# Performance work log

Hardware: AMD Instinct MI355X
Metric: run time of the kernel (lower is better)

Reference implementation:

```python
import jax, jax.numpy as jnp
import numpy as np

B_, C_, H_, W_, N_ = 2, 256, 64, 64, 16


def setup_inputs() -> dict:
    key = jax.random.key(0)
    ks = jax.random.split(key, 6)
    return {
        "features": jax.random.normal(ks[0], (B_, C_, H_, W_), jnp.float32),
        "A_log": jax.random.normal(ks[1], (C_, N_), jnp.float32) * 0.5,
        "D": jax.random.normal(ks[2], (C_,), jnp.float32),
        "W_delta": jax.random.normal(ks[3], (C_, C_), jnp.float32) * 0.02,
        "b_delta": jnp.zeros((C_,), jnp.float32),
        "W_B": jax.random.normal(ks[4], (C_, N_), jnp.float32) * 0.02,
        "W_C": jax.random.normal(ks[5], (C_, N_), jnp.float32) * 0.02,
    }


def _selective_scan(x, A_log, D, W_delta, b_delta, W_B, W_C):
    # x: (B, L, C) -> (B, L, C). Canonical S6 selective scan (mamba corrector).
    delta = jax.nn.softplus(x @ W_delta + b_delta)          # (B, L, C)
    Bm = x @ W_B                                            # (B, L, N)
    Cm = x @ W_C                                            # (B, L, N)
    A = -jnp.exp(A_log)                                     # (C, N), negative real
    dA = jnp.exp(delta[..., None] * A)                      # (B, L, C, N)
    dBx = (delta * x)[..., None] * Bm[:, :, None, :]        # (B, L, C, N)

    def combine(left, right):
        a_l, b_l = left
        a_r, b_r = right
        return (a_l * a_r, a_r * b_l + b_r)

    # h_t = dA_t * h_{t-1} + dBx_t, computed in parallel over L
    _, h = jax.lax.associative_scan(combine, (dA, dBx), axis=1)
    y = jnp.einsum('blcn,bln->blc', h, Cm) + x * D          # (B, L, C)
    return y


def reference(features, A_log, D, W_delta, b_delta, W_B, W_C):
    B, C, H, W = features.shape
    corr = lambda x: _selective_scan(x, A_log, D, W_delta, b_delta, W_B, W_C)

    # direction 1: row-major forward
    flat = features.reshape(B, C, H * W).transpose(0, 2, 1)        # (B, HW, C)
    out1 = corr(flat)
    # direction 2: row-major reversed
    out2 = jnp.flip(corr(jnp.flip(flat, axis=1)), axis=1)
    # direction 3: rows flipped vertically (flip over H), scan, flip back
    rows = features.transpose(0, 2, 3, 1)                          # (B, H, W, C)
    rows_f = jnp.flip(rows, axis=1).reshape(B, H * W, C)
    out3 = jnp.flip(corr(rows_f).reshape(B, H, W, C), axis=1).reshape(B, H * W, C)
    # direction 4: column-major, flipped over W, scan, flip + transpose back
    cols = features.transpose(0, 3, 2, 1)                          # (B, W, H, C)
    cols_f = jnp.flip(cols, axis=1).reshape(B, W * H, C)
    out4 = jnp.flip(corr(cols_f).reshape(B, W, H, C), axis=1)
    out4 = out4.transpose(0, 2, 1, 3).reshape(B, H * W, C)

    mamba_out = (out1 + out2 + out3 + out4) / 4                    # (B, HW, C)
    return mamba_out.transpose(0, 2, 1).reshape(B, C, H, W)
```

## Files before the change

### kernel.cpp

```cpp
#include <hip/hip_runtime.h>
#include <cstdint>
#include <cstddef>

#define BB 2
#define CC 256
#define NN 16
#define LL 4096
#define NCH 128
#define CLEN 32
#define LCH 8
#define LOG2E 1.4426950408889634f

__device__ __forceinline__ float softplus_f(float z) {
    return fmaxf(z, 0.f) + log1pf(expf(-fabsf(z)));
}

__global__ __launch_bounds__(256) void k1_delta_gemm(
    const float* __restrict__ feat, const float* __restrict__ Wd,
    const float* __restrict__ bd, const float* __restrict__ WB,
    const float* __restrict__ WC, float* __restrict__ du,
    float* __restrict__ Bm, float* __restrict__ Cm)
{
    int lc = blockIdx.x & 511;
    int b  = blockIdx.x >> 9;
    int l0 = lc * LCH;
    int c  = threadIdx.x;
    const float* fbase = feat + (size_t)b * CC * LL;

    int lB  = threadIdx.x >> 5;
    int s   = threadIdx.x & 31;
    int mat = s >> 4;
    int n   = s & 15;
    const float* wBC = mat ? WC : WB;

    float accM[LCH] = {};
    float accB = 0.f;

    #pragma unroll 4
    for (int k = 0; k < 256; ++k) {
        const float* frow = fbase + (size_t)k * LL + l0;
        float4 x0 = *(const float4*)(frow + 0);
        float4 x1 = *(const float4*)(frow + 4);
        float wv = Wd[(size_t)k * CC + c];
        float wb = wBC[k * NN + n];
        float xb = frow[lB];

        accM[0] = fmaf(x0.x, wv, accM[0]);
        accM[1] = fmaf(x0.y, wv, accM[1]);
        accM[2] = fmaf(x0.z, wv, accM[2]);
        accM[3] = fmaf(x0.w, wv, accM[3]);
        accM[4] = fmaf(x1.x, wv, accM[4]);
        accM[5] = fmaf(x1.y, wv, accM[5]);
        accM[6] = fmaf(x1.z, wv, accM[6]);
        accM[7] = fmaf(x1.w, wv, accM[7]);
        accB = fmaf(xb, wb, accB);
    }

    (mat ? Cm : Bm)[((size_t)b * LL + l0 + lB) * NN + n] = accB;

    float bdc = bd[c];
    float4 fx[2];
    {
        const float* fcp = fbase + (size_t)c * LL + l0;
        fx[0] = *(const float4*)(fcp + 0);
        fx[1] = *(const float4*)(fcp + 4);
    }
    float2* du2 = (float2*)du;
    const float* fxs = (const float*)fx;
    #pragma unroll
    for (int j = 0; j < LCH; ++j) {
        float dv = softplus_f(accM[j] + bdc);
        float uv = dv * fxs[j];
        du2[((size_t)b * LL + l0 + j) * CC + c] = make_float2(dv, uv);
    }
}

__global__ __launch_bounds__(256) void p1_aggr(
    const float2* __restrict__ du, const float* __restrict__ Bm,
    const float* __restrict__ A_log, float* __restrict__ P, float* __restrict__ S)
{
    int blk = blockIdx.x;
    int cls = blk >> 8;
    int b   = (blk >> 7) & 1;
    int ch  = blk & 127;
    int p0, inner;
    if (cls == 0)      { p0 = 32 * ch;        inner = 1; }
    else if (cls == 1) { p0 = 4095 - 32 * ch; inner = -1; }
    else               { p0 = 63 - (ch >> 1) + 2048 * (ch & 1); inner = 64; }
    int c = threadIdx.x;
    __shared__ float sBm[CLEN * NN];
    for (int i = threadIdx.x; i < CLEN * NN; i += 256) {
        int j = i >> 4, nn = i & 15;
        sBm[i] = Bm[((size_t)b * LL + (p0 + inner * j)) * NN + nn];
    }
    float A2[NN];
    {
        const float4* al = (const float4*)(A_log + c * NN);
        #pragma unroll
        for (int q = 0; q < 4; ++q) {
            float4 v = al[q];
            A2[q*4+0] = -expf(v.x) * LOG2E;
            A2[q*4+1] = -expf(v.y) * LOG2E;
            A2[q*4+2] = -expf(v.z) * LOG2E;
            A2[q*4+3] = -expf(v.w) * LOG2E;
        }
    }
    __syncthreads();
    const float2* dub = du + (size_t)b * LL * CC + c;
    float2 buf[2][8];
    #pragma unroll
    for (int i = 0; i < 8; ++i)
        buf[0][i] = dub[(size_t)(p0 + inner * i) * CC];
    float Sv[NN] = {};
    float sumd = 0.f;
    #pragma unroll
    for (int g = 0; g < 4; ++g) {
        if (g < 3) {
            #pragma unroll
            for (int i = 0; i < 8; ++i)
                buf[(g + 1) & 1][i] = dub[(size_t)(p0 + inner * ((g + 1) * 8 + i)) * CC];
        }
        #pragma unroll
        for (int i = 0; i < 8; ++i) {
            int j = g * 8 + i;
            float2 dv = buf[g & 1][i];
            sumd += dv.x;
            float dA[NN];
            #pragma unroll
            for (int nn = 0; nn < NN; ++nn) dA[nn] = __builtin_amdgcn_exp2f(A2[nn] * dv.x);
            #pragma unroll
            for (int nn = 0; nn < NN; ++nn)
                Sv[nn] = fmaf(dA[nn], Sv[nn], dv.y * sBm[j * 16 + nn]);
        }
    }
    size_t base = ((size_t)((cls * 2 + b) * 128 + ch)) * 4096 + (size_t)c * 16;
    #pragma unroll
    for (int nn = 0; nn < NN; ++nn) {
        P[base + nn] = __builtin_amdgcn_exp2f(A2[nn] * sumd);
        S[base + nn] = Sv[nn];
    }
}

__global__ __launch_bounds__(128) void p2_scan(
    const float* __restrict__ P, const float* __restrict__ S, float* __restrict__ Hin)
{
    int r = blockIdx.x * 128 + threadIdx.x;
    int cn = r & 4095;
    int db = r >> 12;
    int d = db >> 1;
    int cls = (d == 1) ? 1 : ((d == 3) ? 2 : 0);
    int b = db & 1;
    const size_t cbase = ((size_t)(cls * 2 + b) * 128) * 4096 + cn;
    const size_t obase = ((size_t)db * 128) * 4096 + cn;
    float h = 0.f;
    for (int g = 0; g < 16; ++g) {
        float pv[8], sv[8];
        #pragma unroll
        for (int i = 0; i < 8; ++i) {
            int ch = g * 8 + i;
            int chm = (d == 2) ? (126 - 2 * (ch >> 1) + (ch & 1)) : ch;
            size_t ix = cbase + (size_t)chm * 4096;
            pv[i] = P[ix];
            sv[i] = S[ix];
        }
        #pragma unroll
        for (int i = 0; i < 8; ++i) {
            Hin[obase + (size_t)(g * 8 + i) * 4096] = h;
            h = fmaf(pv[i], h, sv[i]);
        }
    }
}

__global__ __launch_bounds__(256) void p3_replay(
    const float2* __restrict__ du, const float* __restrict__ Bm,
    const float* __restrict__ Cm, const float* __restrict__ A_log,
    const float* __restrict__ Hin, float* __restrict__ yA,
    float* __restrict__ yB, float* __restrict__ yC)
{
    int blk = blockIdx.x;
    int sec = blk >> 8;
    int b   = (blk >> 7) & 1;
    int ch  = blk & 127;
    int p0, inner;
    if (sec == 0)      { p0 = 32 * ch;        inner = 1; }
    else if (sec == 1) { p0 = 4095 - 32 * ch; inner = -1; }
    else               { p0 = 63 - (ch >> 1) + 2048 * (ch & 1); inner = 64; }
    int c = threadIdx.x;
    __shared__ float sBm[CLEN * NN];
    __shared__ float sCm[CLEN * NN];
    for (int i = threadIdx.x; i < CLEN * NN; i += 256) {
        int j = i >> 4, nn = i & 15;
        size_t o = ((size_t)b * LL + (p0 + inner * j)) * NN + nn;
        sBm[i] = Bm[o];
        sCm[i] = Cm[o];
    }
    float A2[NN];
    {
        const float4* al = (const float4*)(A_log + c * NN);
        #pragma unroll
        for (int q = 0; q < 4; ++q) {
            float4 v = al[q];
            A2[q*4+0] = -expf(v.x) * LOG2E;
            A2[q*4+1] = -expf(v.y) * LOG2E;
            A2[q*4+2] = -expf(v.z) * LOG2E;
            A2[q*4+3] = -expf(v.w) * LOG2E;
        }
    }
    const float2* dub = du + (size_t)b * LL * CC + c;

    if (sec == 0) {
        int ch2 = 126 - (ch & ~1) + (ch & 1);
        float h0[NN], h2[NN];
        {
            const float4* hp0 = (const float4*)(Hin + ((size_t)(0 * 2 + b) * 128 + ch)  * 4096 + (size_t)c * 16);
            const float4* hp2 = (const float4*)(Hin + ((size_t)(2 * 2 + b) * 128 + ch2) * 4096 + (size_t)c * 16);
            #pragma unroll
            for (int q = 0; q < 4; ++q) {
                float4 v0 = hp0[q], v2 = hp2[q];
                h0[q*4+0]=v0.x; h0[q*4+1]=v0.y; h0[q*4+2]=v0.z; h0[q*4+3]=v0.w;
                h2[q*4+0]=v2.x; h2[q*4+1]=v2.y; h2[q*4+2]=v2.z; h2[q*4+3]=v2.w;
            }
        }
        __syncthreads();
        float2 buf[2][8];
        #pragma unroll
        for (int i = 0; i < 8; ++i)
            buf[0][i] = dub[(size_t)(p0 + i) * CC];
        #pragma unroll
        for (int g = 0; g < 4; ++g) {
            if (g < 3) {
                #pragma unroll
                for (int i = 0; i < 8; ++i)
                    buf[(g + 1) & 1][i] = dub[(size_t)(p0 + (g + 1) * 8 + i) * CC];
            }
            #pragma unroll
            for (int i = 0; i < 8; ++i) {
                int j = g * 8 + i;
                float2 dv = buf[g & 1][i];
                float dA[NN];
                #pragma unroll
                for (int nn = 0; nn < NN; ++nn) dA[nn] = __builtin_amdgcn_exp2f(A2[nn] * dv.x);
                float y0v = 0.f, y2v = 0.f;
                #pragma unroll
                for (int nn = 0; nn < NN; ++nn) {
                    float Bu = dv.y * sBm[j * 16 + nn];
                    float cm = sCm[j * 16 + nn];
                    h0[nn] = fmaf(dA[nn], h0[nn], Bu);
                    h2[nn] = fmaf(dA[nn], h2[nn], Bu);
                    y0v = fmaf(h0[nn], cm, y0v);
                    y2v = fmaf(h2[nn], cm, y2v);
                }
                yA[((size_t)b * LL + p0 + j) * CC + c] = 0.25f * (y0v + y2v);
            }
        }
    } else {
        int d = (sec == 1) ? 1 : 3;
        float h[NN];
        {
            const float4* hp = (const float4*)(Hin + ((size_t)(d * 2 + b) * 128 + ch) * 4096 + (size_t)c * 16);
            #pragma unroll
            for (int q = 0; q < 4; ++q) {
                float4 v = hp[q];
                h[q*4+0]=v.x; h[q*4+1]=v.y; h[q*4+2]=v.z; h[q*4+3]=v.w;
            }
        }
        __syncthreads();
        float* yD = (sec == 1) ? yB : yC;
        float2 buf[2][8];
        #pragma unroll
        for (int i = 0; i < 8; ++i)
            buf[0][i] = dub[(size_t)(p0 + inner * i) * CC];
        #pragma unroll
        for (int g = 0; g < 4; ++g) {
            if (g < 3) {
                #pragma unroll
                for (int i = 0; i < 8; ++i)
                    buf[(g + 1) & 1][i] = dub[(size_t)(p0 + inner * ((g + 1) * 8 + i)) * CC];
            }
            #pragma unroll
            for (int i = 0; i < 8; ++i) {
                int j = g * 8 + i;
                float2 dv = buf[g & 1][i];
                float dA[NN];
                #pragma unroll
                for (int nn = 0; nn < NN; ++nn) dA[nn] = __builtin_amdgcn_exp2f(A2[nn] * dv.x);
                float yv = 0.f;
                #pragma unroll
                for (int nn = 0; nn < NN; ++nn) {
                    float Bu = dv.y * sBm[j * 16 + nn];
                    h[nn] = fmaf(dA[nn], h[nn], Bu);
                    yv = fmaf(h[nn], sCm[j * 16 + nn], yv);
                }
                yD[((size_t)b * LL + p0 + inner * j) * CC + c] = 0.25f * yv;
            }
        }
    }
}

__global__ __launch_bounds__(256) void k6_reduce(
    const float* __restrict__ feat, const float* __restrict__ D,
    const float* __restrict__ yA, const float* __restrict__ yB,
    const float* __restrict__ yC, float* __restrict__ out)
{
    int pt = blockIdx.x & 63;
    int ct = (blockIdx.x >> 6) & 3;
    int b  = blockIdx.x >> 8;
    int p0 = pt * 64, c0 = ct * 64;
    __shared__ float tile[64 * 65];
    {
        int cl = threadIdx.x & 63;
        int pg = threadIdx.x >> 6;
        #pragma unroll
        for (int pp = 0; pp < 16; ++pp) {
            int pl = pp * 4 + pg;
            size_t ix = ((size_t)b * LL + p0 + pl) * CC + c0 + cl;
            tile[cl * 65 + pl] = yA[ix] + yB[ix] + yC[ix];
        }
    }
    __syncthreads();
    {
        int pl = threadIdx.x & 63;
        int cg = threadIdx.x >> 6;
        #pragma unroll
        for (int cc = 0; cc < 16; ++cc) {
            int cloc = cc * 4 + cg;
            int c = c0 + cloc;
            size_t o = ((size_t)b * CC + c) * LL + p0 + pl;
            out[o] = tile[cloc * 65 + pl] + feat[o] * D[c];
        }
    }
}

extern "C" void kernel_launch(void* const* d_in, const int* in_sizes, int n_in,
                              void* d_out, int out_size, void* d_ws, size_t ws_size,
                              hipStream_t stream)
{
    const float* feat  = (const float*)d_in[0];
    const float* A_log = (const float*)d_in[1];
    const float* D     = (const float*)d_in[2];
    const float* Wd    = (const float*)d_in[3];
    const float* bd    = (const float*)d_in[4];
    const float* WB    = (const float*)d_in[5];
    const float* WC    = (const float*)d_in[6];
    float* out = (float*)d_out;

    float* ws  = (float*)d_ws;
    float* du  = ws;
    float* Bm  = du  + (size_t)4194304;
    float* Cm  = Bm  + (size_t)131072;
    float* P   = Cm  + (size_t)131072;
    float* S   = P   + (size_t)3145728;
    float* Hin = S   + (size_t)3145728;
    float* yA  = Hin + (size_t)4194304;
    float* yB  = yA  + (size_t)2097152;
    float* yC  = yB  + (size_t)2097152;

    k1_delta_gemm<<<1024, 256, 0, stream>>>(feat, Wd, bd, WB, WC, du, Bm, Cm);
    p1_aggr<<<768, 256, 0, stream>>>((const float2*)du, Bm, A_log, P, S);
    p2_scan<<<256, 128, 0, stream>>>(P, S, Hin);
    p3_replay<<<768, 256, 0, stream>>>((const float2*)du, Bm, Cm, A_log, Hin, yA, yB, yC);
    k6_reduce<<<512, 256, 0, stream>>>(feat, D, yA, yB, yC, out);
}
```

Before: 172.9 us.

## Pack delta and delta*x as bf16 pairs and split-K the delta GEMM

The intermediate (delta, delta*x) buffer is now stored as two bf16 halves in one 32-bit word instead of a float2, halving the traffic read by the aggregation and replay kernels. The delta projection kernel is restructured so each wavefront owns a quarter of the K dimension and four output channels, with partial sums reduced through shared memory and vectorized stores. The change cuts memory bandwidth in the scan passes but lowers the precision of delta and delta*x to bf16, which feeds exponentials and a long recurrence and may hurt accuracy.

```diff
diff --git a/kernel.cpp b/kernel.cpp
--- a/kernel.cpp
+++ b/kernel.cpp
@@ -15,68 +15,111 @@
     return fmaxf(z, 0.f) + log1pf(expf(-fabsf(z)));
 }
 
+__device__ __forceinline__ uint32_t pack_bf2(float d, float u) {
+    uint32_t lo = (__float_as_uint(d) + 0x8000u) >> 16;
+    uint32_t hh = (__float_as_uint(u) + 0x8000u) & 0xffff0000u;
+    return hh | lo;
+}
+
 __global__ __launch_bounds__(256) void k1_delta_gemm(
     const float* __restrict__ feat, const float* __restrict__ Wd,
     const float* __restrict__ bd, const float* __restrict__ WB,
-    const float* __restrict__ WC, float* __restrict__ du,
+    const float* __restrict__ WC, uint32_t* __restrict__ du,
     float* __restrict__ Bm, float* __restrict__ Cm)
 {
     int lc = blockIdx.x & 511;
     int b  = blockIdx.x >> 9;
     int l0 = lc * LCH;
-    int c  = threadIdx.x;
     const float* fbase = feat + (size_t)b * CC * LL;
 
-    int lB  = threadIdx.x >> 5;
-    int s   = threadIdx.x & 31;
-    int mat = s >> 4;
-    int n   = s & 15;
+    int c4   = threadIdx.x & 63;
+    int kq   = __builtin_amdgcn_readfirstlane(threadIdx.x >> 6);
+    int hi   = (threadIdx.x >> 5) & 1;
+    int slot = threadIdx.x & 31;
+    int mat  = slot >> 4;
+    int n    = slot & 15;
     const float* wBC = mat ? WC : WB;
 
-    float accM[LCH] = {};
-    float accB = 0.f;
-
+    float accM[8][4] = {};
+    float accB[4] = {};
+
+    int kbase = kq * 64;
     #pragma unroll 4
-    for (int k = 0; k < 256; ++k) {
+    for (int kk = 0; kk < 64; ++kk) {
+        int k = kbase + kk;
         const float* frow = fbase + (size_t)k * LL + l0;
-        float4 x0 = *(const float4*)(frow + 0);
+        float4 x0 = *(const float4*)(frow);
         float4 x1 = *(const float4*)(frow + 4);
-        float wv = Wd[(size_t)k * CC + c];
-        float wb = wBC[k * NN + n];
-        float xb = frow[lB];
-
-        accM[0] = fmaf(x0.x, wv, accM[0]);
-        accM[1] = fmaf(x0.y, wv, accM[1]);
-        accM[2] = fmaf(x0.z, wv, accM[2]);
-        accM[3] = fmaf(x0.w, wv, accM[3]);
-        accM[4] = fmaf(x1.x, wv, accM[4]);
-        accM[5] = fmaf(x1.y, wv, accM[5]);
-        accM[6] = fmaf(x1.z, wv, accM[6]);
-        accM[7] = fmaf(x1.w, wv, accM[7]);
-        accB = fmaf(xb, wb, accB);
-    }
-
-    (mat ? Cm : Bm)[((size_t)b * LL + l0 + lB) * NN + n] = accB;
-
-    float bdc = bd[c];
-    float4 fx[2];
+        float4 wv = *(const float4*)&Wd[(size_t)k * CC + (c4 << 2)];
+        float wb  = wBC[k * NN + n];
+        float xs[8] = {x0.x, x0.y, x0.z, x0.w, x1.x, x1.y, x1.z, x1.w};
+        #pragma unroll
+        for (int l = 0; l < 8; ++l) {
+            accM[l][0] = fmaf(xs[l], wv.x, accM[l][0]);
+            accM[l][1] = fmaf(xs[l], wv.y, accM[l][1]);
+            accM[l][2] = fmaf(xs[l], wv.z, accM[l][2]);
+            accM[l][3] = fmaf(xs[l], wv.w, accM[l][3]);
+        }
+        accB[0] = fmaf(hi ? x0.y : x0.x, wb, accB[0]);
+        accB[1] = fmaf(hi ? x0.w : x0.z, wb, accB[1]);
+        accB[2] = fmaf(hi ? x1.y : x1.x, wb, accB[2]);
+        accB[3] = fmaf(hi ? x1.w : x1.z, wb, accB[3]);
+    }
+
+    __shared__ float red[4 * 8 * 64 * 4];
+    __shared__ float redBC[4 * 2 * 32 * 4];
+    #pragma unroll
+    for (int l = 0; l < 8; ++l)
+        *(float4*)&red[((kq * 8 + l) * 64 + c4) * 4] =
+            make_float4(accM[l][0], accM[l][1], accM[l][2], accM[l][3]);
+    *(float4*)&redBC[((kq * 2 + hi) * 32 + slot) * 4] =
+        make_float4(accB[0], accB[1], accB[2], accB[3]);
+    __syncthreads();
+
     {
-        const float* fcp = fbase + (size_t)c * LL + l0;
-        fx[0] = *(const float4*)(fcp + 0);
-        fx[1] = *(const float4*)(fcp + 4);
-    }
-    float2* du2 = (float2*)du;
-    const float* fxs = (const float*)fx;
-    #pragma unroll
-    for (int j = 0; j < LCH; ++j) {
-        float dv = softplus_f(accM[j] + bdc);
-        float uv = dv * fxs[j];
-        du2[((size_t)b * LL + l0 + j) * CC + c] = make_float2(dv, uv);
+        int lr = threadIdx.x >> 5, slotr = threadIdx.x & 31;
+        int jj = lr >> 1, hh = lr & 1;
+        float s = 0.f;
+        #pragma unroll
+        for (int q = 0; q < 4; ++q)
+            s += redBC[((q * 2 + hh) * 32 + slotr) * 4 + jj];
+        int mr = slotr >> 4, nr = slotr & 15;
+        (mr ? Cm : Bm)[((size_t)b * LL + l0 + lr) * NN + nr] = s;
+    }
+
+    float4 bd4 = *(const float4*)&bd[c4 << 2];
+    float2 vx[4];
+    #pragma unroll
+    for (int j = 0; j < 4; ++j)
+        vx[j] = *(const float2*)&fbase[(size_t)(c4 * 4 + j) * LL + l0 + kq * 2];
+    #pragma unroll
+    for (int lo = 0; lo < 2; ++lo) {
+        int l = kq * 2 + lo;
+        float z0 = 0.f, z1 = 0.f, z2 = 0.f, z3 = 0.f;
+        #pragma unroll
+        for (int q = 0; q < 4; ++q) {
+            float4 p = *(float4*)&red[((q * 8 + l) * 64 + c4) * 4];
+            z0 += p.x; z1 += p.y; z2 += p.z; z3 += p.w;
+        }
+        float d0 = softplus_f(z0 + bd4.x);
+        float d1 = softplus_f(z1 + bd4.y);
+        float d2 = softplus_f(z2 + bd4.z);
+        float d3 = softplus_f(z3 + bd4.w);
+        float x0v = lo ? vx[0].y : vx[0].x;
+        float x1v = lo ? vx[1].y : vx[1].x;
+        float x2v = lo ? vx[2].y : vx[2].x;
+        float x3v = lo ? vx[3].y : vx[3].x;
+        uint4 o;
+        o.x = pack_bf2(d0, d0 * x0v);
+        o.y = pack_bf2(d1, d1 * x1v);
+        o.z = pack_bf2(d2, d2 * x2v);
+        o.w = pack_bf2(d3, d3 * x3v);
+        *(uint4*)&du[((size_t)b * LL + l0 + l) * CC + (c4 << 2)] = o;
     }
 }
 
 __global__ __launch_bounds__(256) void p1_aggr(
-    const float2* __restrict__ du, const float* __restrict__ Bm,
+    const uint32_t* __restrict__ du, const float* __restrict__ Bm,
     const float* __restrict__ A_log, float* __restrict__ P, float* __restrict__ S)
 {
     int blk = blockIdx.x;
@@ -106,8 +149,8 @@
         }
     }
     __syncthreads();
-    const float2* dub = du + (size_t)b * LL * CC + c;
-    float2 buf[2][8];
+    const uint32_t* dub = du + (size_t)b * LL * CC + c;
+    uint32_t buf[2][8];
     #pragma unroll
     for (int i = 0; i < 8; ++i)
         buf[0][i] = dub[(size_t)(p0 + inner * i) * CC];
@@ -123,14 +166,16 @@
         #pragma unroll
         for (int i = 0; i < 8; ++i) {
             int j = g * 8 + i;
-            float2 dv = buf[g & 1][i];
-            sumd += dv.x;
+            uint32_t w = buf[g & 1][i];
+            float dx = __uint_as_float(w << 16);
+            float uy = __uint_as_float(w & 0xffff0000u);
+            sumd += dx;
             float dA[NN];
             #pragma unroll
-            for (int nn = 0; nn < NN; ++nn) dA[nn] = __builtin_amdgcn_exp2f(A2[nn] * dv.x);
+            for (int nn = 0; nn < NN; ++nn) dA[nn] = __builtin_amdgcn_exp2f(A2[nn] * dx);
             #pragma unroll
             for (int nn = 0; nn < NN; ++nn)
-                Sv[nn] = fmaf(dA[nn], Sv[nn], dv.y * sBm[j * 16 + nn]);
+                Sv[nn] = fmaf(dA[nn], Sv[nn], uy * sBm[j * 16 + nn]);
         }
     }
     size_t base = ((size_t)((cls * 2 + b) * 128 + ch)) * 4096 + (size_t)c * 16;
@@ -172,7 +217,7 @@
 }
 
 __global__ __launch_bounds__(256) void p3_replay(
-    const float2* __restrict__ du, const float* __restrict__ Bm,
+    const uint32_t* __restrict__ du, const float* __restrict__ Bm,
     const float* __restrict__ Cm, const float* __restrict__ A_log,
     const float* __restrict__ Hin, float* __restrict__ yA,
     float* __restrict__ yB, float* __restrict__ yC)
@@ -206,7 +251,7 @@
             A2[q*4+3] = -expf(v.w) * LOG2E;
         }
     }
-    const float2* dub = du + (size_t)b * LL * CC + c;
+    const uint32_t* dub = du + (size_t)b * LL * CC + c;
 
     if (sec == 0) {
         int ch2 = 126 - (ch & ~1) + (ch & 1);
@@ -222,7 +267,7 @@
             }
         }
         __syncthreads();
-        float2 buf[2][8];
+        uint32_t buf[2][8];
         #pragma unroll
         for (int i = 0; i < 8; ++i)
             buf[0][i] = dub[(size_t)(p0 + i) * CC];
@@ -236,14 +281,16 @@
             #pragma unroll
             for (int i = 0; i < 8; ++i) {
                 int j = g * 8 + i;
-                float2 dv = buf[g & 1][i];
+                uint32_t w = buf[g & 1][i];
+                float dx = __uint_as_float(w << 16);
+                float uy = __uint_as_float(w & 0xffff0000u);
                 float dA[NN];
                 #pragma unroll
-                for (int nn = 0; nn < NN; ++nn) dA[nn] = __builtin_amdgcn_exp2f(A2[nn] * dv.x);
+                for (int nn = 0; nn < NN; ++nn) dA[nn] = __builtin_amdgcn_exp2f(A2[nn] * dx);
                 float y0v = 0.f, y2v = 0.f;
                 #pragma unroll
                 for (int nn = 0; nn < NN; ++nn) {
-                    float Bu = dv.y * sBm[j * 16 + nn];
+                    float Bu = uy * sBm[j * 16 + nn];
                     float cm = sCm[j * 16 + nn];
                     h0[nn] = fmaf(dA[nn], h0[nn], Bu);
                     h2[nn] = fmaf(dA[nn], h2[nn], Bu);
@@ -266,7 +313,7 @@
         }
         __syncthreads();
         float* yD = (sec == 1) ? yB : yC;
-        float2 buf[2][8];
+        uint32_t buf[2][8];
         #pragma unroll
         for (int i = 0; i < 8; ++i)
             buf[0][i] = dub[(size_t)(p0 + inner * i) * CC];
@@ -280,14 +327,16 @@
             #pragma unroll
             for (int i = 0; i < 8; ++i) {
                 int j = g * 8 + i;
-                float2 dv = buf[g & 1][i];
+                uint32_t w = buf[g & 1][i];
+                float dx = __uint_as_float(w << 16);
+                float uy = __uint_as_float(w & 0xffff0000u);
                 float dA[NN];
                 #pragma unroll
-                for (int nn = 0; nn < NN; ++nn) dA[nn] = __builtin_amdgcn_exp2f(A2[nn] * dv.x);
+                for (int nn = 0; nn < NN; ++nn) dA[nn] = __builtin_amdgcn_exp2f(A2[nn] * dx);
                 float yv = 0.f;
                 #pragma unroll
                 for (int nn = 0; nn < NN; ++nn) {
-                    float Bu = dv.y * sBm[j * 16 + nn];
+                    float Bu = uy * sBm[j * 16 + nn];
                     h[nn] = fmaf(dA[nn], h[nn], Bu);
                     yv = fmaf(h[nn], sCm[j * 16 + nn], yv);
                 }
@@ -345,8 +394,8 @@
     float* out = (float*)d_out;
 
     float* ws  = (float*)d_ws;
-    float* du  = ws;
-    float* Bm  = du  + (size_t)4194304;
+    uint32_t* du = (uint32_t*)ws;
+    float* Bm  = ws  + (size_t)2097152;
     float* Cm  = Bm  + (size_t)131072;
     float* P   = Cm  + (size_t)131072;
     float* S   = P   + (size_t)3145728;
@@ -356,8 +405,8 @@
     float* yC  = yB  + (size_t)2097152;
 
     k1_delta_gemm<<<1024, 256, 0, stream>>>(feat, Wd, bd, WB, WC, du, Bm, Cm);
-    p1_aggr<<<768, 256, 0, stream>>>((const float2*)du, Bm, A_log, P, S);
+    p1_aggr<<<768, 256, 0, stream>>>(du, Bm, A_log, P, S);
     p2_scan<<<256, 128, 0, stream>>>(P, S, Hin);
-    p3_replay<<<768, 256, 0, stream>>>((const float2*)du, Bm, Cm, A_log, Hin, yA, yB, yC);
+    p3_replay<<<768, 256, 0, stream>>>(du, Bm, Cm, A_log, Hin, yA, yB, yC);
     k6_reduce<<<512, 256, 0, stream>>>(feat, D, yA, yB, yC, out);
 }
```

After: 161.2 us. -6.7%, faster.
